# Kernel optimization log

Hardware: AMD Instinct MI355X
Metric: run time of the kernel (lower is better)

The kernel has to match this reference:

```python
import jax, jax.numpy as jnp
import numpy as np

N = 50000      # nodes
E = 800000     # edges (before self loops)
F_IN = 64      # n_features
H = 4          # heads
EPS = 1e-5


def _feast_conv(x, src, dst, W, u, c, b, out_ch):
    # FeaStConv (PyG): q_h = softmax_h(u_h^T (x_j - x_i) + c_h);
    # x_i' = mean_{j in N(i)} sum_h q_h * (W_h x_j) + b
    xs = x[src]                                   # [E', Fin]
    xd = x[dst]                                   # [E', Fin]
    q = jax.nn.softmax((xs - xd) @ u + c, axis=-1)          # [E', H]
    m = (xs @ W).reshape(xs.shape[0], H, out_ch)            # [E', H, out]
    msg = jnp.einsum('eh,eho->eo', q, m)                    # [E', out]
    num = jax.ops.segment_sum(msg, dst, num_segments=N)     # [N, out]
    deg = jax.ops.segment_sum(jnp.ones((msg.shape[0],), msg.dtype), dst, num_segments=N)
    return num / jnp.clip(deg, 1.0)[:, None] + b


def setup_inputs() -> dict:
    key = jax.random.key(0)
    ks = jax.random.split(key, 32)
    def gn(k, shape, s=0.1):
        return jax.random.normal(k, shape, jnp.float32) * s
    inp = {
        'x': jax.random.normal(ks[0], (N, F_IN), jnp.float32),
        'edge_index': jax.random.randint(ks[1], (2, E), 0, N),
        # FeaStConv 1: 64 -> 16
        'W1': gn(ks[2], (F_IN, H * 16)), 'u1': gn(ks[3], (F_IN, H)),
        'c1': gn(ks[4], (H,)), 'b1': gn(ks[5], (16,)),
        # FeaStConv 2: 16 -> 32
        'W2': gn(ks[6], (16, H * 32)), 'u2': gn(ks[7], (16, H)),
        'c2': gn(ks[8], (H,)), 'b2': gn(ks[9], (32,)),
        # FeaStConv 3: 32 -> 64
        'W3': gn(ks[10], (32, H * 64)), 'u3': gn(ks[11], (32, H)),
        'c3': gn(ks[12], (H,)), 'b3': gn(ks[13], (64,)),
        # BatchNorm(64) affine params (training-mode batch stats)
        'gamma': jnp.ones((64,), jnp.float32), 'beta': jnp.zeros((64,), jnp.float32),
        # MLP head
        'lw1': gn(ks[14], (64, 32)), 'lb1': gn(ks[15], (32,)),
        'lw2': gn(ks[16], (32, 16)), 'lb2': gn(ks[17], (16,)),
        'lw3': gn(ks[18], (16, 8)),  'lb3': gn(ks[19], (8,)),
        'lw4': gn(ks[20], (8, 4)),   'lb4': gn(ks[21], (4,)),
        'ow':  gn(ks[22], (4, 1)),   'ob':  gn(ks[23], (1,)),
    }
    return inp


def reference(x, edge_index, W1, u1, c1, b1, W2, u2, c2, b2, W3, u3, c3, b3,
              gamma, beta, lw1, lb1, lw2, lb2, lw3, lb3, lw4, lb4, ow, ob):
    # add self loops (PyG FeaStConv default)
    loops = jnp.arange(N, dtype=edge_index.dtype)
    src = jnp.concatenate([edge_index[0], loops])
    dst = jnp.concatenate([edge_index[1], loops])

    h = jax.nn.relu(_feast_conv(x, src, dst, W1, u1, c1, b1, 16))
    h = jax.nn.relu(_feast_conv(h, src, dst, W2, u2, c2, b2, 32))
    h = jax.nn.relu(_feast_conv(h, src, dst, W3, u3, c3, b3, 64))

    # BatchNorm over node dim (training-mode biased batch stats)
    mu = h.mean(axis=0)
    var = h.var(axis=0)
    h = (h - mu) * jax.lax.rsqrt(var + EPS) * gamma + beta

    h = jax.nn.relu(h @ lw1 + lb1)
    h = jax.nn.relu(h @ lw2 + lb2)
    h = jax.nn.relu(h @ lw3 + lb3)
    h = jax.nn.relu(h @ lw4 + lb4)
    return jax.nn.sigmoid(h @ ow + ob)    # [N, 1]
```

## Files before the change

### kernel.cpp

```cpp
#include <hip/hip_runtime.h>

#define NNODES 50000
#define NEDGES 800000
#define SCAN_BLOCKS ((NNODES + 255) / 256)
#define NPART (NNODES / 8)
#define EPS 2048
#define NSLICE ((NEDGES + EPS - 1) / EPS)

__device__ __forceinline__ float4 softq(float4 ss, float4 sd, float4 c4) {
  float l0 = ss.x - sd.x + c4.x;
  float l1 = ss.y - sd.y + c4.y;
  float l2 = ss.z - sd.z + c4.z;
  float l3 = ss.w - sd.w + c4.w;
  float mx = fmaxf(fmaxf(l0, l1), fmaxf(l2, l3));
  float e0 = __expf(l0 - mx), e1 = __expf(l1 - mx);
  float e2 = __expf(l2 - mx), e3 = __expf(l3 - mx);
  float inv = 1.f / (e0 + e1 + e2 + e3);
  return make_float4(e0 * inv, e1 * inv, e2 * inv, e3 * inv);
}

__device__ __forceinline__ void fma4(float4& a, float q, float4 v) {
  a.x += q * v.x; a.y += q * v.y; a.z += q * v.z; a.w += q * v.w;
}
__device__ __forceinline__ float dot4(float4 a, float4 b) {
  return a.x * b.x + a.y * b.y + a.z * b.z + a.w * b.w;
}
__device__ __forceinline__ void st4T(float* ldsT, int k0, int NBp, int nl, float4 v) {
  ldsT[(k0 + 0) * NBp + nl] = v.x;
  ldsT[(k0 + 1) * NBp + nl] = v.y;
  ldsT[(k0 + 2) * NBp + nl] = v.z;
  ldsT[(k0 + 3) * NBp + nl] = v.w;
}
__device__ __forceinline__ float4 shfl4(float4 v, int e, int w) {
  return make_float4(__shfl(v.x, e, w), __shfl(v.y, e, w),
                     __shfl(v.z, e, w), __shfl(v.w, e, w));
}

__global__ __launch_bounds__(256) void hist_kernel(const int* __restrict__ ei,
                                                   int* __restrict__ counts,
                                                   int* __restrict__ rank) {
  int e = blockIdx.x * 256 + threadIdx.x;
  if (e < NEDGES) rank[e] = atomicAdd(&counts[ei[NEDGES + e]], 1);
}

__global__ __launch_bounds__(256) void scanA_kernel(const int* __restrict__ counts,
                                                    int* __restrict__ rowptr,
                                                    int* __restrict__ blockSum) {
  __shared__ int sm[256];
  int i = blockIdx.x * 256 + threadIdx.x;
  int v = (i < NNODES) ? counts[i] : 0;
  sm[threadIdx.x] = v;
  __syncthreads();
  for (int off = 1; off < 256; off <<= 1) {
    int x = (threadIdx.x >= off) ? sm[threadIdx.x - off] : 0;
    __syncthreads();
    sm[threadIdx.x] += x;
    __syncthreads();
  }
  if (i < NNODES) rowptr[i] = sm[threadIdx.x] - v;
  if (threadIdx.x == 255) blockSum[blockIdx.x] = sm[255];
}

__global__ __launch_bounds__(256) void scanB_kernel(int* __restrict__ blockSum,
                                                    int* __restrict__ blockOff) {
  __shared__ int sm[256];
  int v = (threadIdx.x < SCAN_BLOCKS) ? blockSum[threadIdx.x] : 0;
  sm[threadIdx.x] = v;
  __syncthreads();
  for (int off = 1; off < 256; off <<= 1) {
    int x = (threadIdx.x >= off) ? sm[threadIdx.x - off] : 0;
    __syncthreads();
    sm[threadIdx.x] += x;
    __syncthreads();
  }
  if (threadIdx.x < SCAN_BLOCKS) blockOff[threadIdx.x] = sm[threadIdx.x] - v;
}

__global__ __launch_bounds__(256) void scanC_kernel(int* __restrict__ rowptr,
                                                    const int* __restrict__ blockOff) {
  int i = blockIdx.x * 256 + threadIdx.x;
  if (i < NNODES) rowptr[i] += blockOff[blockIdx.x];
  if (i == 0) rowptr[NNODES] = NEDGES;
}

__global__ __launch_bounds__(256) void scatter_kernel(const int* __restrict__ ei,
                                                      const int* __restrict__ rowptr,
                                                      const int* __restrict__ rank,
                                                      int* __restrict__ col) {
  const int p = blockIdx.x & 7;
  const int sl = blockIdx.x >> 3;
  const int P0 = p * NPART;
  const int e1 = min((sl + 1) * EPS, NEDGES);
  for (int e = sl * EPS + threadIdx.x; e < e1; e += 256) {
    int dst = __builtin_nontemporal_load(&ei[NEDGES + e]);
    if ((unsigned)(dst - P0) < (unsigned)NPART) {
      int pos = rowptr[dst] + __builtin_nontemporal_load(&rank[e]);
      col[pos] = __builtin_nontemporal_load(&ei[e]);
    }
  }
}

__global__ __launch_bounds__(256) void prep_kernel(const float* __restrict__ W1,
                                                   const float* __restrict__ W2,
                                                   const float* __restrict__ W3,
                                                   float* __restrict__ Wk1,
                                                   float* __restrict__ Wk2,
                                                   float* __restrict__ Wk3) {
  int i = blockIdx.x * 256 + threadIdx.x;
  if (i < 4096) {
    int f = i >> 6, j = i & 63;
    Wk1[i] = W1[f * 64 + ((j & 3) << 4) + (j >> 2)];
  } else if (i < 6144) {
    int i2 = i - 4096;
    int k = i2 >> 5, o = i2 & 31;
    int hh = k >> 4, f = k & 15;
    Wk2[i2] = W2[f * 128 + hh * 32 + o];
  } else if (i < 14336) {
    int i3 = i - 6144;
    int k = i3 >> 6, o = i3 & 63;
    int hh = k >> 5, f = k & 31;
    Wk3[i3] = W3[f * 256 + hh * 64 + o];
  }
}

template<int K, int OUTT, int MO, bool DEGBIAS>
__global__ __launch_bounds__(256) void ngemm_kernel(const float* __restrict__ A,
                                                    const float* __restrict__ Wk,
                                                    const int* __restrict__ rowptr,
                                                    const float* __restrict__ bptr,
                                                    float* __restrict__ C) {
  constexpr int OG = OUTT / MO;
  constexpr int NB = 256 / OG;
  constexpr int NBp = NB + 1;
  __shared__ float ldsT[K * NBp];
  const int tid = threadIdx.x;
  const int nb0 = blockIdx.x * NB;
  for (int i = tid; i < NB * (K / 4); i += 256) {
    int r = i / (K / 4), kq = i - r * (K / 4);
    int n = nb0 + r;
    if (n >= NNODES) n = NNODES - 1;
    float4 v = ((const float4*)A)[n * (K / 4) + kq];
    st4T(ldsT, kq << 2, NBp, r, v);
  }
  __syncthreads();
  const int o0 = __builtin_amdgcn_readfirstlane(tid / NB) * MO;
  const int nl = tid & (NB - 1);
  const int n = nb0 + nl;
  float acc[MO];
#pragma unroll
  for (int m = 0; m < MO; ++m) acc[m] = 0.f;
#pragma unroll 4
  for (int k = 0; k < K; ++k) {
    float a = ldsT[k * NBp + nl];
    const float* wr = Wk + k * OUTT + o0;
#pragma unroll
    for (int m = 0; m < MO; ++m) acc[m] += a * wr[m];
  }
  if (n < NNODES) {
    float sc = 1.f;
    if (DEGBIAS) sc = 1.f / (float)(rowptr[n + 1] - rowptr[n] + 1);
#pragma unroll
    for (int m4 = 0; m4 < MO / 4; ++m4) {
      float4 v;
      if (DEGBIAS) {
        v.x = fmaxf(acc[m4 * 4 + 0] * sc + bptr[o0 + m4 * 4 + 0], 0.f);
        v.y = fmaxf(acc[m4 * 4 + 1] * sc + bptr[o0 + m4 * 4 + 1], 0.f);
        v.z = fmaxf(acc[m4 * 4 + 2] * sc + bptr[o0 + m4 * 4 + 2], 0.f);
        v.w = fmaxf(acc[m4 * 4 + 3] * sc + bptr[o0 + m4 * 4 + 3], 0.f);
      } else {
        v = make_float4(acc[m4 * 4 + 0], acc[m4 * 4 + 1],
                        acc[m4 * 4 + 2], acc[m4 * 4 + 3]);
      }
      ((float4*)C)[n * (OUTT / 4) + (o0 >> 2) + m4] = v;
    }
  }
}

template<int FIN, int OUTT, int MO>
__global__ __launch_bounds__(256) void fusedG_kernel(const int* __restrict__ rowptr,
                                                     const int* __restrict__ col,
                                                     const float* __restrict__ s,
                                                     const float* __restrict__ x,
                                                     const float* __restrict__ Wk,
                                                     const float* __restrict__ cptr,
                                                     const float* __restrict__ bptr,
                                                     float* __restrict__ h) {
  constexpr int LPN = FIN / 8;
  constexpr int NB = 256 / LPN;
  constexpr int NBp = NB + 1;
  constexpr int K = 4 * FIN;
  constexpr int OG = OUTT / MO;
  static_assert(OG == 256 / NB, "geometry mismatch");
  __shared__ float ldsT[K * NBp];
  const int tid = threadIdx.x;
  const int nb0 = blockIdx.x * NB;
  const float4* sF4 = (const float4*)s;
  const float4* xF4 = (const float4*)x;

  {
    const int lane = tid & (LPN - 1);
    const int sub = tid / LPN;
    int n = nb0 + sub;
    if (n >= NNODES) n = NNODES - 1;
    float4 c4 = *(const float4*)cptr;
    float mxc = fmaxf(fmaxf(c4.x, c4.y), fmaxf(c4.z, c4.w));
    float4 qsl = make_float4(__expf(c4.x - mxc), __expf(c4.y - mxc),
                             __expf(c4.z - mxc), __expf(c4.w - mxc));
    float sinv = 1.f / (qsl.x + qsl.y + qsl.z + qsl.w);
    qsl.x *= sinv; qsl.y *= sinv; qsl.z *= sinv; qsl.w *= sinv;
    float4 sd = sF4[n];
    const float4* xn = xF4 + n * (FIN / 4) + 2 * lane;
    float4 xa = xn[0], xb = xn[1];
    float4 g0a = make_float4(qsl.x * xa.x, qsl.x * xa.y, qsl.x * xa.z, qsl.x * xa.w);
    float4 g0b = make_float4(qsl.x * xb.x, qsl.x * xb.y, qsl.x * xb.z, qsl.x * xb.w);
    float4 g1a = make_float4(qsl.y * xa.x, qsl.y * xa.y, qsl.y * xa.z, qsl.y * xa.w);
    float4 g1b = make_float4(qsl.y * xb.x, qsl.y * xb.y, qsl.y * xb.z, qsl.y * xb.w);
    float4 g2a = make_float4(qsl.z * xa.x, qsl.z * xa.y, qsl.z * xa.z, qsl.z * xa.w);
    float4 g2b = make_float4(qsl.z * xb.x, qsl.z * xb.y, qsl.z * xb.z, qsl.z * xb.w);
    float4 g3a = make_float4(qsl.w * xa.x, qsl.w * xa.y, qsl.w * xa.z, qsl.w * xa.w);
    float4 g3b = make_float4(qsl.w * xb.x, qsl.w * xb.y, qsl.w * xb.z, qsl.w * xb.w);
    const int beg = rowptr[n], end = rowptr[n + 1];
    int idx = beg;
    for (; idx + LPN <= end; idx += LPN) {
      int myS = col[idx + lane];
      float4 qL = softq(sF4[myS], sd, c4);
#pragma unroll
      for (int e = 0; e < LPN; ++e) {
        int srcE = __shfl(myS, e, LPN);
        float4 q = shfl4(qL, e, LPN);
        const float4* xr = xF4 + srcE * (FIN / 4) + 2 * lane;
        float4 x0a = xr[0], x0b = xr[1];
        fma4(g0a, q.x, x0a); fma4(g0b, q.x, x0b);
        fma4(g1a, q.y, x0a); fma4(g1b, q.y, x0b);
        fma4(g2a, q.z, x0a); fma4(g2b, q.z, x0b);
        fma4(g3a, q.w, x0a); fma4(g3b, q.w, x0b);
      }
    }
    for (; idx < end; ++idx) {
      int s0 = col[idx];
      float4 qv = softq(sF4[s0], sd, c4);
      const float4* xr = xF4 + s0 * (FIN / 4) + 2 * lane;
      float4 x0a = xr[0], x0b = xr[1];
      fma4(g0a, qv.x, x0a); fma4(g0b, qv.x, x0b);
      fma4(g1a, qv.y, x0a); fma4(g1b, qv.y, x0b);
      fma4(g2a, qv.z, x0a); fma4(g2b, qv.z, x0b);
      fma4(g3a, qv.w, x0a); fma4(g3b, qv.w, x0b);
    }
    const int f0 = 8 * lane;
    st4T(ldsT, 0 * FIN + f0, NBp, sub, g0a); st4T(ldsT, 0 * FIN + f0 + 4, NBp, sub, g0b);
    st4T(ldsT, 1 * FIN + f0, NBp, sub, g1a); st4T(ldsT, 1 * FIN + f0 + 4, NBp, sub, g1b);
    st4T(ldsT, 2 * FIN + f0, NBp, sub, g2a); st4T(ldsT, 2 * FIN + f0 + 4, NBp, sub, g2b);
    st4T(ldsT, 3 * FIN + f0, NBp, sub, g3a); st4T(ldsT, 3 * FIN + f0 + 4, NBp, sub, g3b);
  }
  __syncthreads();

  const int o0 = __builtin_amdgcn_readfirstlane(tid / NB) * MO;
  const int nl = tid & (NB - 1);
  const int n = nb0 + nl;
  float acc[MO];
#pragma unroll
  for (int m = 0; m < MO; ++m) acc[m] = 0.f;
#pragma unroll 4
  for (int k = 0; k < K; ++k) {
    float a = ldsT[k * NBp + nl];
    const float* wr = Wk + k * OUTT + o0;
#pragma unroll
    for (int m = 0; m < MO; ++m) acc[m] += a * wr[m];
  }
  if (n < NNODES) {
    float sc = 1.f / (float)(rowptr[n + 1] - rowptr[n] + 1);
#pragma unroll
    for (int m4 = 0; m4 < MO / 4; ++m4) {
      float4 v;
      v.x = fmaxf(acc[m4 * 4 + 0] * sc + bptr[o0 + m4 * 4 + 0], 0.f);
      v.y = fmaxf(acc[m4 * 4 + 1] * sc + bptr[o0 + m4 * 4 + 1], 0.f);
      v.z = fmaxf(acc[m4 * 4 + 2] * sc + bptr[o0 + m4 * 4 + 2], 0.f);
      v.w = fmaxf(acc[m4 * 4 + 3] * sc + bptr[o0 + m4 * 4 + 3], 0.f);
      ((float4*)h)[n * (OUTT / 4) + (o0 >> 2) + m4] = v;
    }
  }
}

template<int FIN>
__global__ __launch_bounds__(256) void s_kernel(const float* __restrict__ x,
                                                const float* __restrict__ u,
                                                float* __restrict__ s) {
  int tid = blockIdx.x * 256 + threadIdx.x;
  int n = tid >> 2, h = tid & 3;
  if (n >= NNODES) return;
  const float4* xr = (const float4*)x + n * (FIN / 4);
  float acc = 0.f;
#pragma unroll
  for (int f4 = 0; f4 < FIN / 4; ++f4) {
    float4 xv = xr[f4];
    acc += xv.x * u[(4 * f4 + 0) * 4 + h] + xv.y * u[(4 * f4 + 1) * 4 + h] +
           xv.z * u[(4 * f4 + 2) * 4 + h] + xv.w * u[(4 * f4 + 3) * 4 + h];
  }
  s[tid] = acc;
}

__global__ __launch_bounds__(256) void gather1_kernel(const int* __restrict__ rowptr,
                                                      const int* __restrict__ col,
                                                      const float* __restrict__ s,
                                                      const float* __restrict__ t,
                                                      const float* __restrict__ cptr,
                                                      const float* __restrict__ bptr,
                                                      float* __restrict__ h) {
  const int lane = threadIdx.x & 7;
  const int sub = threadIdx.x >> 3;
  const int n = blockIdx.x * 32 + sub;
  if (n >= NNODES) return;
  const float4* sF4 = (const float4*)s;
  const float4* tF4 = (const float4*)t;
  float4 c4 = *(const float4*)cptr;
  float mxc = fmaxf(fmaxf(c4.x, c4.y), fmaxf(c4.z, c4.w));
  float4 qs = make_float4(__expf(c4.x - mxc), __expf(c4.y - mxc),
                          __expf(c4.z - mxc), __expf(c4.w - mxc));
  float sinv = 1.f / (qs.x + qs.y + qs.z + qs.w);
  qs.x *= sinv; qs.y *= sinv; qs.z *= sinv; qs.w *= sinv;
  float4 sd = sF4[n];
  const float4* trow = tF4 + n * 16 + 2 * lane;
  float acc0 = dot4(qs, trow[0]);
  float acc1 = dot4(qs, trow[1]);
  const int beg = rowptr[n], end = rowptr[n + 1];
  int idx = beg;
  for (; idx + 8 <= end; idx += 8) {
    int myS = col[idx + lane];
    float4 qL = softq(sF4[myS], sd, c4);
#pragma unroll
    for (int e = 0; e < 8; ++e) {
      int srcE = __shfl(myS, e, 8);
      float4 q = shfl4(qL, e, 8);
      const float4* tw = tF4 + srcE * 16 + 2 * lane;
      acc0 += dot4(q, tw[0]);
      acc1 += dot4(q, tw[1]);
    }
  }
  for (; idx < end; ++idx) {
    int src = col[idx];
    float4 qv = softq(sF4[src], sd, c4);
    const float4* tw = tF4 + src * 16 + 2 * lane;
    acc0 += dot4(qv, tw[0]);
    acc1 += dot4(qv, tw[1]);
  }
  float d = 1.f / (float)(end - beg + 1);
  h[n * 16 + 2 * lane + 0] = fmaxf(acc0 * d + bptr[2 * lane + 0], 0.f);
  h[n * 16 + 2 * lane + 1] = fmaxf(acc1 * d + bptr[2 * lane + 1], 0.f);
}

__global__ __launch_bounds__(256) void stats_kernel(const float* __restrict__ h3,
                                                    float* __restrict__ sums) {
  const int o = threadIdx.x & 63;
  const int r = threadIdx.x >> 6;
  float accS = 0.f, accQ = 0.f;
  for (int base = blockIdx.x * 4; base < NNODES; base += gridDim.x * 4) {
    int n = base + r;
    if (n < NNODES) {
      float v = h3[n * 64 + o];
      accS += v;
      accQ += v * v;
    }
  }
  __shared__ float ls[256], lq[256];
  ls[threadIdx.x] = accS;
  lq[threadIdx.x] = accQ;
  __syncthreads();
  if (threadIdx.x < 64) {
    float a = ls[threadIdx.x] + ls[threadIdx.x + 64] + ls[threadIdx.x + 128] + ls[threadIdx.x + 192];
    float qq = lq[threadIdx.x] + lq[threadIdx.x + 64] + lq[threadIdx.x + 128] + lq[threadIdx.x + 192];
    atomicAdd(&sums[threadIdx.x], a);
    atomicAdd(&sums[64 + threadIdx.x], qq);
  }
}

__global__ __launch_bounds__(256) void mlp_kernel(
    const float* __restrict__ h3, const float* __restrict__ sums,
    const float* __restrict__ gamma, const float* __restrict__ beta,
    const float* __restrict__ lw1, const float* __restrict__ lb1,
    const float* __restrict__ lw2, const float* __restrict__ lb2,
    const float* __restrict__ lw3, const float* __restrict__ lb3,
    const float* __restrict__ lw4, const float* __restrict__ lb4,
    const float* __restrict__ ow, const float* __restrict__ ob,
    float* __restrict__ out) {
  __shared__ float w1[64 * 32], w2[32 * 16], w3[16 * 8], w4[8 * 4];
  __shared__ float b1s[32], b2s[16], b3s[8], b4s[4], wos[4];
  __shared__ float scale[64], shift[64];
  int tid = threadIdx.x;
  for (int i = tid; i < 64 * 32; i += 256) w1[i] = lw1[i];
  for (int i = tid; i < 32 * 16; i += 256) w2[i] = lw2[i];
  if (tid < 128) w3[tid] = lw3[tid];
  if (tid < 32) { w4[tid] = lw4[tid]; b1s[tid] = lb1[tid]; }
  if (tid < 16) b2s[tid] = lb2[tid];
  if (tid < 8) b3s[tid] = lb3[tid];
  if (tid < 4) { b4s[tid] = lb4[tid]; wos[tid] = ow[tid]; }
  if (tid < 64) {
    float mu = sums[tid] * (1.f / NNODES);
    float var = sums[64 + tid] * (1.f / NNODES) - mu * mu;
    float sc = rsqrtf(var + 1e-5f) * gamma[tid];
    scale[tid] = sc;
    shift[tid] = beta[tid] - mu * sc;
  }
  __syncthreads();
  int n = blockIdx.x * 256 + tid;
  if (n >= NNODES) return;
  float obv = ob[0];
  const float4* hr = (const float4*)h3 + n * 16;
  float z1[32];
#pragma unroll
  for (int j = 0; j < 32; ++j) z1[j] = b1s[j];
  for (int i4 = 0; i4 < 16; ++i4) {
    float4 hv = hr[i4];
    float a0 = hv.x * scale[4 * i4 + 0] + shift[4 * i4 + 0];
    float a1 = hv.y * scale[4 * i4 + 1] + shift[4 * i4 + 1];
    float a2 = hv.z * scale[4 * i4 + 2] + shift[4 * i4 + 2];
    float a3 = hv.w * scale[4 * i4 + 3] + shift[4 * i4 + 3];
#pragma unroll
    for (int j = 0; j < 32; ++j) {
      z1[j] += a0 * w1[(4 * i4 + 0) * 32 + j] + a1 * w1[(4 * i4 + 1) * 32 + j] +
               a2 * w1[(4 * i4 + 2) * 32 + j] + a3 * w1[(4 * i4 + 3) * 32 + j];
    }
  }
  float z2[16];
#pragma unroll
  for (int j = 0; j < 16; ++j) z2[j] = b2s[j];
  for (int i = 0; i < 32; ++i) {
    float a = fmaxf(z1[i], 0.f);
#pragma unroll
    for (int j = 0; j < 16; ++j) z2[j] += a * w2[i * 16 + j];
  }
  float z3[8];
#pragma unroll
  for (int j = 0; j < 8; ++j) z3[j] = b3s[j];
  for (int i = 0; i < 16; ++i) {
    float a = fmaxf(z2[i], 0.f);
#pragma unroll
    for (int j = 0; j < 8; ++j) z3[j] += a * w3[i * 8 + j];
  }
  float z4[4];
#pragma unroll
  for (int j = 0; j < 4; ++j) z4[j] = b4s[j];
  for (int i = 0; i < 8; ++i) {
    float a = fmaxf(z3[i], 0.f);
#pragma unroll
    for (int j = 0; j < 4; ++j) z4[j] += a * w4[i * 4 + j];
  }
  float zo = obv;
#pragma unroll
  for (int i = 0; i < 4; ++i) zo += fmaxf(z4[i], 0.f) * wos[i];
  out[n] = 1.f / (1.f + __expf(-zo));
}

extern "C" void kernel_launch(void* const* d_in, const int* in_sizes, int n_in,
                              void* d_out, int out_size, void* d_ws, size_t ws_size,
                              hipStream_t stream) {
  const float* x  = (const float*)d_in[0];
  const int*   ei = (const int*)d_in[1];
  const float* W1 = (const float*)d_in[2];  const float* u1 = (const float*)d_in[3];
  const float* c1 = (const float*)d_in[4];  const float* b1 = (const float*)d_in[5];
  const float* W2 = (const float*)d_in[6];  const float* u2 = (const float*)d_in[7];
  const float* c2 = (const float*)d_in[8];  const float* b2 = (const float*)d_in[9];
  const float* W3 = (const float*)d_in[10]; const float* u3 = (const float*)d_in[11];
  const float* c3 = (const float*)d_in[12]; const float* b3 = (const float*)d_in[13];
  const float* gamma = (const float*)d_in[14]; const float* beta = (const float*)d_in[15];
  const float* lw1 = (const float*)d_in[16]; const float* lb1 = (const float*)d_in[17];
  const float* lw2 = (const float*)d_in[18]; const float* lb2 = (const float*)d_in[19];
  const float* lw3 = (const float*)d_in[20]; const float* lb3 = (const float*)d_in[21];
  const float* lw4 = (const float*)d_in[22]; const float* lb4 = (const float*)d_in[23];
  const float* ow  = (const float*)d_in[24]; const float* ob  = (const float*)d_in[25];
  float* out = (float*)d_out;

  float* t    = (float*)d_ws;
  float* hA   = t + (size_t)NNODES * 64;
  float* hB   = hA + (size_t)NNODES * 64;
  float* s    = hB + (size_t)NNODES * 64;
  float* sums = s + (size_t)NNODES * 4;
  float* Wk1  = sums + 128;
  float* Wk2  = Wk1 + 4096;
  float* Wk3  = Wk2 + 2048;
  int*   rowptr   = (int*)(Wk3 + 8192);
  int*   counts   = rowptr + NNODES + 8;
  int*   blockSum = counts + NNODES;
  int*   blockOff = blockSum + 256;
  int*   col      = blockOff + 256;
  int*   rank     = col + NEDGES;

  hipMemsetAsync(counts, 0, NNODES * sizeof(int), stream);
  hipMemsetAsync(sums, 0, 128 * sizeof(float), stream);

  prep_kernel<<<56, 256, 0, stream>>>(W1, W2, W3, Wk1, Wk2, Wk3);
  hist_kernel<<<(NEDGES + 255) / 256, 256, 0, stream>>>(ei, counts, rank);
  scanA_kernel<<<SCAN_BLOCKS, 256, 0, stream>>>(counts, rowptr, blockSum);
  scanB_kernel<<<1, 256, 0, stream>>>(blockSum, blockOff);
  scanC_kernel<<<SCAN_BLOCKS, 256, 0, stream>>>(rowptr, blockOff);
  scatter_kernel<<<NSLICE * 8, 256, 0, stream>>>(ei, rowptr, rank, col);

  ngemm_kernel<64, 64, 16, false><<<(NNODES + 63) / 64, 256, 0, stream>>>(x, Wk1, nullptr, nullptr, t);
  s_kernel<64><<<(NNODES * 4 + 255) / 256, 256, 0, stream>>>(x, u1, s);
  gather1_kernel<<<(NNODES + 31) / 32, 256, 0, stream>>>(rowptr, col, s, t, c1, b1, hA);

  s_kernel<16><<<(NNODES * 4 + 255) / 256, 256, 0, stream>>>(hA, u2, s);
  fusedG_kernel<16, 32, 16><<<(NNODES + 127) / 128, 256, 0, stream>>>(rowptr, col, s, hA, Wk2, c2, b2, hB);

  s_kernel<32><<<(NNODES * 4 + 255) / 256, 256, 0, stream>>>(hB, u3, s);
  fusedG_kernel<32, 64, 16><<<(NNODES + 63) / 64, 256, 0, stream>>>(rowptr, col, s, hB, Wk3, c3, b3, hA);

  stats_kernel<<<256, 256, 0, stream>>>(hA, sums);
  mlp_kernel<<<(NNODES + 255) / 256, 256, 0, stream>>>(hA, sums, gamma, beta, lw1, lb1,
                                                       lw2, lb2, lw3, lb3, lw4, lb4,
                                                       ow, ob, out);
}
```

Baseline: 242.1 us.

## Use 16-bit CSR indices, merge scan passes, fuse BatchNorm stats into last conv

```diff
diff --git a/kernel.cpp b/kernel.cpp
--- a/kernel.cpp
+++ b/kernel.cpp
@@ -6,6 +6,8 @@
 #define NPART (NNODES / 8)
 #define EPS 2048
 #define NSLICE ((NEDGES + EPS - 1) / EPS)
+
+typedef unsigned short u16;
 
 __device__ __forceinline__ float4 softq(float4 ss, float4 sd, float4 c4) {
   float l0 = ss.x - sd.x + c4.x;
@@ -38,9 +40,9 @@
 
 __global__ __launch_bounds__(256) void hist_kernel(const int* __restrict__ ei,
                                                    int* __restrict__ counts,
-                                                   int* __restrict__ rank) {
+                                                   u16* __restrict__ rank) {
   int e = blockIdx.x * 256 + threadIdx.x;
-  if (e < NEDGES) rank[e] = atomicAdd(&counts[ei[NEDGES + e]], 1);
+  if (e < NEDGES) rank[e] = (u16)atomicAdd(&counts[ei[NEDGES + e]], 1);
 }
 
 __global__ __launch_bounds__(256) void scanA_kernel(const int* __restrict__ counts,
@@ -61,8 +63,8 @@
   if (threadIdx.x == 255) blockSum[blockIdx.x] = sm[255];
 }
 
-__global__ __launch_bounds__(256) void scanB_kernel(int* __restrict__ blockSum,
-                                                    int* __restrict__ blockOff) {
+__global__ __launch_bounds__(256) void scanBC_kernel(const int* __restrict__ blockSum,
+                                                     int* __restrict__ rowptr) {
   __shared__ int sm[256];
   int v = (threadIdx.x < SCAN_BLOCKS) ? blockSum[threadIdx.x] : 0;
   sm[threadIdx.x] = v;
@@ -73,20 +75,16 @@
     sm[threadIdx.x] += x;
     __syncthreads();
   }
-  if (threadIdx.x < SCAN_BLOCKS) blockOff[threadIdx.x] = sm[threadIdx.x] - v;
-}
-
-__global__ __launch_bounds__(256) void scanC_kernel(int* __restrict__ rowptr,
-                                                    const int* __restrict__ blockOff) {
+  int off = (blockIdx.x == 0) ? 0 : sm[blockIdx.x - 1];
   int i = blockIdx.x * 256 + threadIdx.x;
-  if (i < NNODES) rowptr[i] += blockOff[blockIdx.x];
+  if (i < NNODES) rowptr[i] += off;
   if (i == 0) rowptr[NNODES] = NEDGES;
 }
 
 __global__ __launch_bounds__(256) void scatter_kernel(const int* __restrict__ ei,
                                                       const int* __restrict__ rowptr,
-                                                      const int* __restrict__ rank,
-                                                      int* __restrict__ col) {
+                                                      const u16* __restrict__ rank,
+                                                      u16* __restrict__ col) {
   const int p = blockIdx.x & 7;
   const int sl = blockIdx.x >> 3;
   const int P0 = p * NPART;
@@ -94,8 +92,8 @@
   for (int e = sl * EPS + threadIdx.x; e < e1; e += 256) {
     int dst = __builtin_nontemporal_load(&ei[NEDGES + e]);
     if ((unsigned)(dst - P0) < (unsigned)NPART) {
-      int pos = rowptr[dst] + __builtin_nontemporal_load(&rank[e]);
-      col[pos] = __builtin_nontemporal_load(&ei[e]);
+      int pos = rowptr[dst] + (int)__builtin_nontemporal_load(&rank[e]);
+      col[pos] = (u16)__builtin_nontemporal_load(&ei[e]);
     }
   }
 }
@@ -123,11 +121,9 @@
   }
 }
 
-template<int K, int OUTT, int MO, bool DEGBIAS>
+template<int K, int OUTT, int MO>
 __global__ __launch_bounds__(256) void ngemm_kernel(const float* __restrict__ A,
                                                     const float* __restrict__ Wk,
-                                                    const int* __restrict__ rowptr,
-                                                    const float* __restrict__ bptr,
                                                     float* __restrict__ C) {
   constexpr int OG = OUTT / MO;
   constexpr int NB = 256 / OG;
@@ -157,34 +153,25 @@
     for (int m = 0; m < MO; ++m) acc[m] += a * wr[m];
   }
   if (n < NNODES) {
-    float sc = 1.f;
-    if (DEGBIAS) sc = 1.f / (float)(rowptr[n + 1] - rowptr[n] + 1);
 #pragma unroll
     for (int m4 = 0; m4 < MO / 4; ++m4) {
-      float4 v;
-      if (DEGBIAS) {
-        v.x = fmaxf(acc[m4 * 4 + 0] * sc + bptr[o0 + m4 * 4 + 0], 0.f);
-        v.y = fmaxf(acc[m4 * 4 + 1] * sc + bptr[o0 + m4 * 4 + 1], 0.f);
-        v.z = fmaxf(acc[m4 * 4 + 2] * sc + bptr[o0 + m4 * 4 + 2], 0.f);
-        v.w = fmaxf(acc[m4 * 4 + 3] * sc + bptr[o0 + m4 * 4 + 3], 0.f);
-      } else {
-        v = make_float4(acc[m4 * 4 + 0], acc[m4 * 4 + 1],
-                        acc[m4 * 4 + 2], acc[m4 * 4 + 3]);
-      }
+      float4 v = make_float4(acc[m4 * 4 + 0], acc[m4 * 4 + 1],
+                             acc[m4 * 4 + 2], acc[m4 * 4 + 3]);
       ((float4*)C)[n * (OUTT / 4) + (o0 >> 2) + m4] = v;
     }
   }
 }
 
-template<int FIN, int OUTT, int MO>
+template<int FIN, int OUTT, int MO, bool STATS>
 __global__ __launch_bounds__(256) void fusedG_kernel(const int* __restrict__ rowptr,
-                                                     const int* __restrict__ col,
+                                                     const u16* __restrict__ col,
                                                      const float* __restrict__ s,
                                                      const float* __restrict__ x,
                                                      const float* __restrict__ Wk,
                                                      const float* __restrict__ cptr,
                                                      const float* __restrict__ bptr,
-                                                     float* __restrict__ h) {
+                                                     float* __restrict__ h,
+                                                     float* __restrict__ sums) {
   constexpr int LPN = FIN / 8;
   constexpr int NB = 256 / LPN;
   constexpr int NBp = NB + 1;
@@ -222,7 +209,7 @@
     const int beg = rowptr[n], end = rowptr[n + 1];
     int idx = beg;
     for (; idx + LPN <= end; idx += LPN) {
-      int myS = col[idx + lane];
+      int myS = (int)col[idx + lane];
       float4 qL = softq(sF4[myS], sd, c4);
 #pragma unroll
       for (int e = 0; e < LPN; ++e) {
@@ -237,7 +224,7 @@
       }
     }
     for (; idx < end; ++idx) {
-      int s0 = col[idx];
+      int s0 = (int)col[idx];
       float4 qv = softq(sF4[s0], sd, c4);
       const float4* xr = xF4 + s0 * (FIN / 4) + 2 * lane;
       float4 x0a = xr[0], x0b = xr[1];
@@ -267,6 +254,9 @@
 #pragma unroll
     for (int m = 0; m < MO; ++m) acc[m] += a * wr[m];
   }
+  float sS[MO], sQ[MO];
+#pragma unroll
+  for (int m = 0; m < MO; ++m) { sS[m] = 0.f; sQ[m] = 0.f; }
   if (n < NNODES) {
     float sc = 1.f / (float)(rowptr[n + 1] - rowptr[n] + 1);
 #pragma unroll
@@ -277,6 +267,27 @@
       v.z = fmaxf(acc[m4 * 4 + 2] * sc + bptr[o0 + m4 * 4 + 2], 0.f);
       v.w = fmaxf(acc[m4 * 4 + 3] * sc + bptr[o0 + m4 * 4 + 3], 0.f);
       ((float4*)h)[n * (OUTT / 4) + (o0 >> 2) + m4] = v;
+      if (STATS) {
+        sS[m4 * 4 + 0] = v.x; sQ[m4 * 4 + 0] = v.x * v.x;
+        sS[m4 * 4 + 1] = v.y; sQ[m4 * 4 + 1] = v.y * v.y;
+        sS[m4 * 4 + 2] = v.z; sQ[m4 * 4 + 2] = v.z * v.z;
+        sS[m4 * 4 + 3] = v.w; sQ[m4 * 4 + 3] = v.w * v.w;
+      }
+    }
+  }
+  if (STATS) {
+#pragma unroll
+    for (int m = 0; m < MO; ++m) {
+      float a = sS[m], q = sQ[m];
+#pragma unroll
+      for (int off = 1; off < 64; off <<= 1) {
+        a += __shfl_xor(a, off);
+        q += __shfl_xor(q, off);
+      }
+      if ((tid & 63) == 0) {
+        atomicAdd(&sums[o0 + m], a);
+        atomicAdd(&sums[64 + o0 + m], q);
+      }
     }
   }
 }
@@ -300,7 +311,7 @@
 }
 
 __global__ __launch_bounds__(256) void gather1_kernel(const int* __restrict__ rowptr,
-                                                      const int* __restrict__ col,
+                                                      const u16* __restrict__ col,
                                                       const float* __restrict__ s,
                                                       const float* __restrict__ t,
                                                       const float* __restrict__ cptr,
@@ -325,7 +336,7 @@
   const int beg = rowptr[n], end = rowptr[n + 1];
   int idx = beg;
   for (; idx + 8 <= end; idx += 8) {
-    int myS = col[idx + lane];
+    int myS = (int)col[idx + lane];
     float4 qL = softq(sF4[myS], sd, c4);
 #pragma unroll
     for (int e = 0; e < 8; ++e) {
@@ -337,7 +348,7 @@
     }
   }
   for (; idx < end; ++idx) {
-    int src = col[idx];
+    int src = (int)col[idx];
     float4 qv = softq(sF4[src], sd, c4);
     const float4* tw = tF4 + src * 16 + 2 * lane;
     acc0 += dot4(qv, tw[0]);
@@ -346,31 +357,6 @@
   float d = 1.f / (float)(end - beg + 1);
   h[n * 16 + 2 * lane + 0] = fmaxf(acc0 * d + bptr[2 * lane + 0], 0.f);
   h[n * 16 + 2 * lane + 1] = fmaxf(acc1 * d + bptr[2 * lane + 1], 0.f);
-}
-
-__global__ __launch_bounds__(256) void stats_kernel(const float* __restrict__ h3,
-                                                    float* __restrict__ sums) {
-  const int o = threadIdx.x & 63;
-  const int r = threadIdx.x >> 6;
-  float accS = 0.f, accQ = 0.f;
-  for (int base = blockIdx.x * 4; base < NNODES; base += gridDim.x * 4) {
-    int n = base + r;
-    if (n < NNODES) {
-      float v = h3[n * 64 + o];
-      accS += v;
-      accQ += v * v;
-    }
-  }
-  __shared__ float ls[256], lq[256];
-  ls[threadIdx.x] = accS;
-  lq[threadIdx.x] = accQ;
-  __syncthreads();
-  if (threadIdx.x < 64) {
-    float a = ls[threadIdx.x] + ls[threadIdx.x + 64] + ls[threadIdx.x + 128] + ls[threadIdx.x + 192];
-    float qq = lq[threadIdx.x] + lq[threadIdx.x + 64] + lq[threadIdx.x + 128] + lq[threadIdx.x + 192];
-    atomicAdd(&sums[threadIdx.x], a);
-    atomicAdd(&sums[64 + threadIdx.x], qq);
-  }
 }
 
 __global__ __launch_bounds__(256) void mlp_kernel(
@@ -480,9 +466,8 @@
   int*   rowptr   = (int*)(Wk3 + 8192);
   int*   counts   = rowptr + NNODES + 8;
   int*   blockSum = counts + NNODES;
-  int*   blockOff = blockSum + 256;
-  int*   col      = blockOff + 256;
-  int*   rank     = col + NEDGES;
+  u16*   col      = (u16*)(blockSum + 256);
+  u16*   rank     = col + NEDGES;
 
   hipMemsetAsync(counts, 0, NNODES * sizeof(int), stream);
   hipMemsetAsync(sums, 0, 128 * sizeof(float), stream);
@@ -490,21 +475,21 @@
   prep_kernel<<<56, 256, 0, stream>>>(W1, W2, W3, Wk1, Wk2, Wk3);
   hist_kernel<<<(NEDGES + 255) / 256, 256, 0, stream>>>(ei, counts, rank);
   scanA_kernel<<<SCAN_BLOCKS, 256, 0, stream>>>(counts, rowptr, blockSum);
-  scanB_kernel<<<1, 256, 0, stream>>>(blockSum, blockOff);
-  scanC_kernel<<<SCAN_BLOCKS, 256, 0, stream>>>(rowptr, blockOff);
+  scanBC_kernel<<<SCAN_BLOCKS, 256, 0, stream>>>(blockSum, rowptr);
   scatter_kernel<<<NSLICE * 8, 256, 0, stream>>>(ei, rowptr, rank, col);
 
-  ngemm_kernel<64, 64, 16, false><<<(NNODES + 63) / 64, 256, 0, stream>>>(x, Wk1, nullptr, nullptr, t);
+  ngemm_kernel<64, 64, 16><<<(NNODES + 63) / 64, 256, 0, stream>>>(x, Wk1, t);
   s_kernel<64><<<(NNODES * 4 + 255) / 256, 256, 0, stream>>>(x, u1, s);
   gather1_kernel<<<(NNODES + 31) / 32, 256, 0, stream>>>(rowptr, col, s, t, c1, b1, hA);
 
   s_kernel<16><<<(NNODES * 4 + 255) / 256, 256, 0, stream>>>(hA, u2, s);
-  fusedG_kernel<16, 32, 16><<<(NNODES + 127) / 128, 256, 0, stream>>>(rowptr, col, s, hA, Wk2, c2, b2, hB);
+  fusedG_kernel<16, 32, 16, false><<<(NNODES + 127) / 128, 256, 0, stream>>>(
+      rowptr, col, s, hA, Wk2, c2, b2, hB, nullptr);
 
   s_kernel<32><<<(NNODES * 4 + 255) / 256, 256, 0, stream>>>(hB, u3, s);
-  fusedG_kernel<32, 64, 16><<<(NNODES + 63) / 64, 256, 0, stream>>>(rowptr, col, s, hB, Wk3, c3, b3, hA);
-
-  stats_kernel<<<256, 256, 0, stream>>>(hA, sums);
+  fusedG_kernel<32, 64, 16, true><<<(NNODES + 63) / 64, 256, 0, stream>>>(
+      rowptr, col, s, hB, Wk3, c3, b3, hA, sums);
+
   mlp_kernel<<<(NNODES + 255) / 256, 256, 0, stream>>>(hA, sums, gamma, beta, lw1, lb1,
                                                        lw2, lb2, lw3, lb3, lw4, lb4,
                                                        ow, ob, out);
```

Result: slower. 516.9 us (+113.5%).
